# Kernel tuning notes

Measured on AMD Instinct MI355X. Metric: run time of the kernel, lower is better.

Reference implementation:

```python
import jax, jax.numpy as jnp
import numpy as np


def setup_inputs() -> dict:
    key = jax.random.key(0)
    ks = jax.random.split(key, 6)
    B, N, D, C = 16, 4096, 1024, 4
    bags = jax.random.normal(ks[0], (B, N, D), dtype=jnp.float32)
    query = jax.random.normal(ks[1], (D,), dtype=jnp.float32)
    W1 = jax.random.normal(ks[2], (3 * D, 512), dtype=jnp.float32) * 0.02
    b1 = jax.random.normal(ks[3], (512,), dtype=jnp.float32) * 0.02
    W2 = jax.random.normal(ks[4], (512, C), dtype=jnp.float32) * 0.02
    b2 = jax.random.normal(ks[5], (C,), dtype=jnp.float32) * 0.02
    return {"bags": bags, "query": query, "W1": W1, "b1": b1, "W2": W2, "b2": b2}


def reference(bags, query, W1, b1, W2, b2):
    # bags: [B, N, D] instance features (frozen feat_extractor output)
    mean_pool = jnp.mean(bags, axis=1)                     # [B, D]
    max_pool = jnp.max(bags, axis=1)                       # [B, D]
    # attention pooling: softmax over instances of <bag_i, query>
    scores = jax.nn.softmax(jnp.einsum('bnd,d->bn', bags, query), axis=1)  # [B, N]
    attn_pool = jnp.einsum('bn,bnd->bd', scores, bags)     # [B, D]
    x = jnp.concatenate([mean_pool, max_pool, attn_pool], axis=-1)  # [B, 3D]
    x = x @ W1 + b1
    x = x @ W2 + b2
    return x
```

## Files before the change

kernel.cpp:

```cpp
#include <hip/hip_runtime.h>
#include <math.h>

#define BNUM 16
#define NNUM 4096
#define DNUM 1024
#define CNUM 4
#define HNUM 512

#define SCH   64
#define ROWS  (NNUM / SCH)
#define RPW   (ROWS / 4)

#define PSTRIDE 3080
#define NPART   (BNUM * SCH)
#define XOFF    ((size_t)NPART * PSTRIDE)
#define WOFF    (XOFF + (size_t)BNUM * 3 * DNUM)

#define NEG_INF (-__builtin_inff())

__global__ __launch_bounds__(256) void k_mainpass(const float* __restrict__ bags,
                                                  const float* __restrict__ query,
                                                  float* __restrict__ ws) {
    const int chunk = blockIdx.x;
    const int b     = blockIdx.y;
    const int tid   = threadIdx.x;
    const int wave  = tid >> 6;
    const int lane  = tid & 63;

    const float4* q4 = (const float4*)query;
    float4 q[4];
#pragma unroll
    for (int s = 0; s < 4; ++s) q[s] = q4[s * 64 + lane];

    float4 sum[4], mx[4], acc[4];
#pragma unroll
    for (int s = 0; s < 4; ++s) {
        sum[s] = make_float4(0.f, 0.f, 0.f, 0.f);
        acc[s] = make_float4(0.f, 0.f, 0.f, 0.f);
        mx[s]  = make_float4(NEG_INF, NEG_INF, NEG_INF, NEG_INF);
    }
    float m = NEG_INF, l = 0.f;

    const int n0 = chunk * ROWS + wave * RPW;
    const float4* base = (const float4*)(bags + (size_t)b * NNUM * DNUM);

    for (int r = 0; r < RPW; ++r) {
        const float4* row = base + (size_t)(n0 + r) * (DNUM / 4);
        float4 v[4];
#pragma unroll
        for (int s = 0; s < 4; ++s) v[s] = row[s * 64 + lane];

        float pd = 0.f;
#pragma unroll
        for (int s = 0; s < 4; ++s)
            pd += v[s].x * q[s].x + v[s].y * q[s].y + v[s].z * q[s].z + v[s].w * q[s].w;
#pragma unroll
        for (int off = 32; off; off >>= 1) pd += __shfl_xor(pd, off, 64);

        const float mnew  = fmaxf(m, pd);
        const float alpha = __expf(m - mnew);
        const float w     = __expf(pd - mnew);
        l = l * alpha + w;
        m = mnew;

#pragma unroll
        for (int s = 0; s < 4; ++s) {
            sum[s].x += v[s].x; sum[s].y += v[s].y; sum[s].z += v[s].z; sum[s].w += v[s].w;
            mx[s].x = fmaxf(mx[s].x, v[s].x); mx[s].y = fmaxf(mx[s].y, v[s].y);
            mx[s].z = fmaxf(mx[s].z, v[s].z); mx[s].w = fmaxf(mx[s].w, v[s].w);
            acc[s].x = acc[s].x * alpha + w * v[s].x;
            acc[s].y = acc[s].y * alpha + w * v[s].y;
            acc[s].z = acc[s].z * alpha + w * v[s].z;
            acc[s].w = acc[s].w * alpha + w * v[s].w;
        }
    }

    __shared__ float buf[4][DNUM];
    __shared__ float sm[4], sl[4];
    if (lane == 0) { sm[wave] = m; sl[wave] = l; }

    float* wsp = ws + (size_t)(b * SCH + chunk) * PSTRIDE;

#pragma unroll
    for (int s = 0; s < 4; ++s) ((float4*)(&buf[wave][s * 256]))[lane] = sum[s];
    __syncthreads();
    {
        float4 a0 = ((float4*)buf[0])[tid];
        float4 a1 = ((float4*)buf[1])[tid];
        float4 a2 = ((float4*)buf[2])[tid];
        float4 a3 = ((float4*)buf[3])[tid];
        float4 r;
        r.x = a0.x + a1.x + a2.x + a3.x;
        r.y = a0.y + a1.y + a2.y + a3.y;
        r.z = a0.z + a1.z + a2.z + a3.z;
        r.w = a0.w + a1.w + a2.w + a3.w;
        ((float4*)wsp)[tid] = r;
    }
    __syncthreads();

#pragma unroll
    for (int s = 0; s < 4; ++s) ((float4*)(&buf[wave][s * 256]))[lane] = mx[s];
    __syncthreads();
    {
        float4 a0 = ((float4*)buf[0])[tid];
        float4 a1 = ((float4*)buf[1])[tid];
        float4 a2 = ((float4*)buf[2])[tid];
        float4 a3 = ((float4*)buf[3])[tid];
        float4 r;
        r.x = fmaxf(fmaxf(a0.x, a1.x), fmaxf(a2.x, a3.x));
        r.y = fmaxf(fmaxf(a0.y, a1.y), fmaxf(a2.y, a3.y));
        r.z = fmaxf(fmaxf(a0.z, a1.z), fmaxf(a2.z, a3.z));
        r.w = fmaxf(fmaxf(a0.w, a1.w), fmaxf(a2.w, a3.w));
        ((float4*)(wsp + 1024))[tid] = r;
    }
    __syncthreads();

#pragma unroll
    for (int s = 0; s < 4; ++s) ((float4*)(&buf[wave][s * 256]))[lane] = acc[s];
    __syncthreads();
    {
        const float m0 = sm[0], m1 = sm[1], m2 = sm[2], m3 = sm[3];
        const float mb = fmaxf(fmaxf(m0, m1), fmaxf(m2, m3));
        const float e0 = __expf(m0 - mb), e1 = __expf(m1 - mb);
        const float e2 = __expf(m2 - mb), e3 = __expf(m3 - mb);
        float4 a0 = ((float4*)buf[0])[tid];
        float4 a1 = ((float4*)buf[1])[tid];
        float4 a2 = ((float4*)buf[2])[tid];
        float4 a3 = ((float4*)buf[3])[tid];
        float4 r;
        r.x = a0.x * e0 + a1.x * e1 + a2.x * e2 + a3.x * e3;
        r.y = a0.y * e0 + a1.y * e1 + a2.y * e2 + a3.y * e3;
        r.z = a0.z * e0 + a1.z * e1 + a2.z * e2 + a3.z * e3;
        r.w = a0.w * e0 + a1.w * e1 + a2.w * e2 + a3.w * e3;
        ((float4*)(wsp + 2048))[tid] = r;
        if (tid == 0) {
            wsp[3072] = mb;
            wsp[3073] = sl[0] * e0 + sl[1] * e1 + sl[2] * e2 + sl[3] * e3;
        }
    }
}

__global__ __launch_bounds__(64) void k_combine(float* __restrict__ ws) {
    const int b = blockIdx.x;
    const int d = blockIdx.y * 64 + threadIdx.x;
    const float* pb = ws + (size_t)b * SCH * PSTRIDE;

    float mb = NEG_INF;
    for (int c = 0; c < SCH; ++c) mb = fmaxf(mb, pb[(size_t)c * PSTRIDE + 3072]);
    float lb = 0.f;
    for (int c = 0; c < SCH; ++c)
        lb += pb[(size_t)c * PSTRIDE + 3073] * __expf(pb[(size_t)c * PSTRIDE + 3072] - mb);

    float s = 0.f, mxv = NEG_INF, av = 0.f;
    for (int c = 0; c < SCH; ++c) {
        const float* p = pb + (size_t)c * PSTRIDE;
        s += p[d];
        mxv = fmaxf(mxv, p[1024 + d]);
        av += p[2048 + d] * __expf(p[3072] - mb);
    }
    float* x = ws + XOFF + (size_t)b * 3 * DNUM;
    x[d]            = s * (1.f / NNUM);
    x[DNUM + d]     = mxv;
    x[2 * DNUM + d] = av / lb;
}

__global__ __launch_bounds__(256) void k_weff(const float* __restrict__ W1,
                                              const float* __restrict__ W2,
                                              float* __restrict__ ws) {
    const int tid  = threadIdx.x;
    const int wave = tid >> 6, lane = tid & 63;
    const int k    = blockIdx.x * 4 + wave;
    const float*  r  = W1 + (size_t)k * HNUM;
    const float4* w2 = (const float4*)W2;

    float a0 = 0.f, a1 = 0.f, a2 = 0.f, a3 = 0.f;
#pragma unroll
    for (int t = 0; t < 8; ++t) {
        const int j = lane * 8 + t;
        const float  wv = r[j];
        const float4 w  = w2[j];
        a0 += wv * w.x; a1 += wv * w.y; a2 += wv * w.z; a3 += wv * w.w;
    }
#pragma unroll
    for (int off = 32; off; off >>= 1) {
        a0 += __shfl_xor(a0, off, 64);
        a1 += __shfl_xor(a1, off, 64);
        a2 += __shfl_xor(a2, off, 64);
        a3 += __shfl_xor(a3, off, 64);
    }
    if (lane == 0)
        ((float4*)(ws + WOFF))[k] = make_float4(a0, a1, a2, a3);
}

__global__ __launch_bounds__(256) void k_head(const float* __restrict__ b1,
                                              const float* __restrict__ b2,
                                              const float* __restrict__ W2,
                                              const float* __restrict__ ws,
                                              float* __restrict__ out) {
    const int i   = blockIdx.x;
    const int tid = threadIdx.x;
    const float*  x    = ws + XOFF + (size_t)i * 3 * DNUM;
    const float4* weff = (const float4*)(ws + WOFF);
    const float4* w2   = (const float4*)W2;

    float a0 = 0.f, a1 = 0.f, a2 = 0.f, a3 = 0.f;
    for (int k = tid; k < 3 * DNUM; k += 256) {
        const float  xv = x[k];
        const float4 w  = weff[k];
        a0 += xv * w.x; a1 += xv * w.y; a2 += xv * w.z; a3 += xv * w.w;
    }
    for (int j = tid; j < HNUM; j += 256) {
        const float  bv = b1[j];
        const float4 w  = w2[j];
        a0 += bv * w.x; a1 += bv * w.y; a2 += bv * w.z; a3 += bv * w.w;
    }
#pragma unroll
    for (int off = 32; off; off >>= 1) {
        a0 += __shfl_xor(a0, off, 64);
        a1 += __shfl_xor(a1, off, 64);
        a2 += __shfl_xor(a2, off, 64);
        a3 += __shfl_xor(a3, off, 64);
    }
    __shared__ float red[4][4];
    const int wave = tid >> 6, lane = tid & 63;
    if (lane == 0) { red[wave][0] = a0; red[wave][1] = a1; red[wave][2] = a2; red[wave][3] = a3; }
    __syncthreads();
    if (tid < 4) {
        out[i * 4 + tid] = red[0][tid] + red[1][tid] + red[2][tid] + red[3][tid] + b2[tid];
    }
}

extern "C" void kernel_launch(void* const* d_in, const int* in_sizes, int n_in,
                              void* d_out, int out_size, void* d_ws, size_t ws_size,
                              hipStream_t stream) {
    const float* bags  = (const float*)d_in[0];
    const float* query = (const float*)d_in[1];
    const float* W1    = (const float*)d_in[2];
    const float* b1    = (const float*)d_in[3];
    const float* W2    = (const float*)d_in[4];
    const float* b2    = (const float*)d_in[5];
    float* out = (float*)d_out;
    float* ws  = (float*)d_ws;

    k_weff    <<<(3 * DNUM) / 4,        256, 0, stream>>>(W1, W2, ws);
    k_mainpass<<<dim3(SCH, BNUM),       256, 0, stream>>>(bags, query, ws);
    k_combine <<<dim3(BNUM, DNUM / 64),  64, 0, stream>>>(ws);
    k_head    <<<BNUM,                  256, 0, stream>>>(b1, b2, W2, ws, out);
}
```

Before: 405.1 us.

## Process two rows per iteration with lazy rescale; fuse combine and head kernels

The main pass now loads two rows per iteration and rescales the online-softmax accumulators only when the running max increases. This raises memory-level parallelism and removes per-row exp and multiply work. The separate combine and head kernels are merged into one k_finish kernel that reduces the partials and applies the folded weights, saving a launch and a workspace round trip. The b1·W2+b2 bias is precomputed in an extra k_weff block. The fused finish kernel uses only 16 blocks, so its per-bag reduction is less parallel than the old 256-block combine.

```diff
diff --git a/kernel.cpp b/kernel.cpp
--- a/kernel.cpp
+++ b/kernel.cpp
@@ -15,6 +15,7 @@
 #define NPART   (BNUM * SCH)
 #define XOFF    ((size_t)NPART * PSTRIDE)
 #define WOFF    (XOFF + (size_t)BNUM * 3 * DNUM)
+#define BIASOFF (WOFF + (size_t)3 * DNUM * 4)
 
 #define NEG_INF (-__builtin_inff())
 
@@ -44,34 +45,56 @@
     const int n0 = chunk * ROWS + wave * RPW;
     const float4* base = (const float4*)(bags + (size_t)b * NNUM * DNUM);
 
-    for (int r = 0; r < RPW; ++r) {
-        const float4* row = base + (size_t)(n0 + r) * (DNUM / 4);
-        float4 v[4];
-#pragma unroll
-        for (int s = 0; s < 4; ++s) v[s] = row[s * 64 + lane];
-
-        float pd = 0.f;
-#pragma unroll
-        for (int s = 0; s < 4; ++s)
-            pd += v[s].x * q[s].x + v[s].y * q[s].y + v[s].z * q[s].z + v[s].w * q[s].w;
-#pragma unroll
-        for (int off = 32; off; off >>= 1) pd += __shfl_xor(pd, off, 64);
-
-        const float mnew  = fmaxf(m, pd);
-        const float alpha = __expf(m - mnew);
-        const float w     = __expf(pd - mnew);
-        l = l * alpha + w;
-        m = mnew;
-
+    for (int r = 0; r < RPW; r += 2) {
+        const float4* rowA = base + (size_t)(n0 + r) * (DNUM / 4);
+        const float4* rowB = rowA + (DNUM / 4);
+        float4 va[4], vb[4];
+#pragma unroll
+        for (int s = 0; s < 4; ++s) va[s] = rowA[s * 64 + lane];
+#pragma unroll
+        for (int s = 0; s < 4; ++s) vb[s] = rowB[s * 64 + lane];
+
+        float pa = 0.f, pb = 0.f;
 #pragma unroll
         for (int s = 0; s < 4; ++s) {
-            sum[s].x += v[s].x; sum[s].y += v[s].y; sum[s].z += v[s].z; sum[s].w += v[s].w;
-            mx[s].x = fmaxf(mx[s].x, v[s].x); mx[s].y = fmaxf(mx[s].y, v[s].y);
-            mx[s].z = fmaxf(mx[s].z, v[s].z); mx[s].w = fmaxf(mx[s].w, v[s].w);
-            acc[s].x = acc[s].x * alpha + w * v[s].x;
-            acc[s].y = acc[s].y * alpha + w * v[s].y;
-            acc[s].z = acc[s].z * alpha + w * v[s].z;
-            acc[s].w = acc[s].w * alpha + w * v[s].w;
+            pa += va[s].x * q[s].x + va[s].y * q[s].y + va[s].z * q[s].z + va[s].w * q[s].w;
+            pb += vb[s].x * q[s].x + vb[s].y * q[s].y + vb[s].z * q[s].z + vb[s].w * q[s].w;
+        }
+#pragma unroll
+        for (int off = 32; off; off >>= 1) {
+            pa += __shfl_xor(pa, off, 64);
+            pb += __shfl_xor(pb, off, 64);
+        }
+
+        const float mnew = fmaxf(m, fmaxf(pa, pb));
+        if (mnew > m) {
+            const float alpha = __expf(m - mnew);
+            l *= alpha;
+#pragma unroll
+            for (int s = 0; s < 4; ++s) {
+                acc[s].x *= alpha; acc[s].y *= alpha;
+                acc[s].z *= alpha; acc[s].w *= alpha;
+            }
+            m = mnew;
+        }
+        const float wa = __expf(pa - m);
+        const float wb = __expf(pb - m);
+        l += wa + wb;
+
+#pragma unroll
+        for (int s = 0; s < 4; ++s) {
+            sum[s].x += va[s].x + vb[s].x;
+            sum[s].y += va[s].y + vb[s].y;
+            sum[s].z += va[s].z + vb[s].z;
+            sum[s].w += va[s].w + vb[s].w;
+            mx[s].x = fmaxf(mx[s].x, fmaxf(va[s].x, vb[s].x));
+            mx[s].y = fmaxf(mx[s].y, fmaxf(va[s].y, vb[s].y));
+            mx[s].z = fmaxf(mx[s].z, fmaxf(va[s].z, vb[s].z));
+            mx[s].w = fmaxf(mx[s].w, fmaxf(va[s].w, vb[s].w));
+            acc[s].x += wa * va[s].x + wb * vb[s].x;
+            acc[s].y += wa * va[s].y + wb * vb[s].y;
+            acc[s].z += wa * va[s].z + wb * vb[s].z;
+            acc[s].w += wa * va[s].w + wb * vb[s].w;
         }
     }
 
@@ -140,93 +163,138 @@
     }
 }
 
-__global__ __launch_bounds__(64) void k_combine(float* __restrict__ ws) {
-    const int b = blockIdx.x;
-    const int d = blockIdx.y * 64 + threadIdx.x;
-    const float* pb = ws + (size_t)b * SCH * PSTRIDE;
-
-    float mb = NEG_INF;
-    for (int c = 0; c < SCH; ++c) mb = fmaxf(mb, pb[(size_t)c * PSTRIDE + 3072]);
-    float lb = 0.f;
-    for (int c = 0; c < SCH; ++c)
-        lb += pb[(size_t)c * PSTRIDE + 3073] * __expf(pb[(size_t)c * PSTRIDE + 3072] - mb);
-
-    float s = 0.f, mxv = NEG_INF, av = 0.f;
-    for (int c = 0; c < SCH; ++c) {
-        const float* p = pb + (size_t)c * PSTRIDE;
-        s += p[d];
-        mxv = fmaxf(mxv, p[1024 + d]);
-        av += p[2048 + d] * __expf(p[3072] - mb);
-    }
-    float* x = ws + XOFF + (size_t)b * 3 * DNUM;
-    x[d]            = s * (1.f / NNUM);
-    x[DNUM + d]     = mxv;
-    x[2 * DNUM + d] = av / lb;
-}
-
 __global__ __launch_bounds__(256) void k_weff(const float* __restrict__ W1,
                                               const float* __restrict__ W2,
+                                              const float* __restrict__ b1,
+                                              const float* __restrict__ b2,
                                               float* __restrict__ ws) {
     const int tid  = threadIdx.x;
     const int wave = tid >> 6, lane = tid & 63;
-    const int k    = blockIdx.x * 4 + wave;
-    const float*  r  = W1 + (size_t)k * HNUM;
     const float4* w2 = (const float4*)W2;
 
-    float a0 = 0.f, a1 = 0.f, a2 = 0.f, a3 = 0.f;
-#pragma unroll
-    for (int t = 0; t < 8; ++t) {
-        const int j = lane * 8 + t;
-        const float  wv = r[j];
-        const float4 w  = w2[j];
-        a0 += wv * w.x; a1 += wv * w.y; a2 += wv * w.z; a3 += wv * w.w;
+    if (blockIdx.x < 768) {
+        const int k = blockIdx.x * 4 + wave;
+        const float* r = W1 + (size_t)k * HNUM;
+        float a0 = 0.f, a1 = 0.f, a2 = 0.f, a3 = 0.f;
+#pragma unroll
+        for (int t = 0; t < 8; ++t) {
+            const int j = lane * 8 + t;
+            const float  wv = r[j];
+            const float4 w  = w2[j];
+            a0 += wv * w.x; a1 += wv * w.y; a2 += wv * w.z; a3 += wv * w.w;
+        }
+#pragma unroll
+        for (int off = 32; off; off >>= 1) {
+            a0 += __shfl_xor(a0, off, 64);
+            a1 += __shfl_xor(a1, off, 64);
+            a2 += __shfl_xor(a2, off, 64);
+            a3 += __shfl_xor(a3, off, 64);
+        }
+        if (lane == 0)
+            ((float4*)(ws + WOFF))[k] = make_float4(a0, a1, a2, a3);
+    } else if (wave == 0) {
+        float a0 = 0.f, a1 = 0.f, a2 = 0.f, a3 = 0.f;
+#pragma unroll
+        for (int t = 0; t < 8; ++t) {
+            const int j = lane * 8 + t;
+            const float  bv = b1[j];
+            const float4 w  = w2[j];
+            a0 += bv * w.x; a1 += bv * w.y; a2 += bv * w.z; a3 += bv * w.w;
+        }
+#pragma unroll
+        for (int off = 32; off; off >>= 1) {
+            a0 += __shfl_xor(a0, off, 64);
+            a1 += __shfl_xor(a1, off, 64);
+            a2 += __shfl_xor(a2, off, 64);
+            a3 += __shfl_xor(a3, off, 64);
+        }
+        if (lane == 0) {
+            float* bias = ws + BIASOFF;
+            bias[0] = a0 + b2[0];
+            bias[1] = a1 + b2[1];
+            bias[2] = a2 + b2[2];
+            bias[3] = a3 + b2[3];
+        }
+    }
+}
+
+__global__ __launch_bounds__(256) void k_finish(const float* __restrict__ ws,
+                                                float* __restrict__ out) {
+    const int b    = blockIdx.x;
+    const int tid  = threadIdx.x;
+    const int wave = tid >> 6, lane = tid & 63;
+
+    __shared__ float eS[SCH];
+    __shared__ float lbS;
+    __shared__ float red[4][4];
+
+    const float* pb = ws + (size_t)b * SCH * PSTRIDE;
+
+    if (wave == 0) {
+        const float* p = pb + (size_t)lane * PSTRIDE;
+        const float mlane = p[3072];
+        const float llane = p[3073];
+        float mb = mlane;
+#pragma unroll
+        for (int off = 32; off; off >>= 1) mb = fmaxf(mb, __shfl_xor(mb, off, 64));
+        const float e = __expf(mlane - mb);
+        float lb = llane * e;
+#pragma unroll
+        for (int off = 32; off; off >>= 1) lb += __shfl_xor(lb, off, 64);
+        eS[lane] = e;
+        if (lane == 0) lbS = lb;
+    }
+    __syncthreads();
+    const float inv_lb = 1.f / lbS;
+
+    float4 s  = make_float4(0.f, 0.f, 0.f, 0.f);
+    float4 a  = make_float4(0.f, 0.f, 0.f, 0.f);
+    float4 mxv = make_float4(NEG_INF, NEG_INF, NEG_INF, NEG_INF);
+    for (int c = 0; c < SCH; ++c) {
+        const float* p = pb + (size_t)c * PSTRIDE;
+        const float4 sv = ((const float4*)p)[tid];
+        const float4 mv = ((const float4*)(p + 1024))[tid];
+        const float4 av = ((const float4*)(p + 2048))[tid];
+        const float e = eS[c];
+        s.x += sv.x; s.y += sv.y; s.z += sv.z; s.w += sv.w;
+        mxv.x = fmaxf(mxv.x, mv.x); mxv.y = fmaxf(mxv.y, mv.y);
+        mxv.z = fmaxf(mxv.z, mv.z); mxv.w = fmaxf(mxv.w, mv.w);
+        a.x += e * av.x; a.y += e * av.y; a.z += e * av.z; a.w += e * av.w;
+    }
+
+    const float4* weff = (const float4*)(ws + WOFF);
+    float c0 = 0.f, c1 = 0.f, c2 = 0.f, c3 = 0.f;
+    const float scm = 1.f / NNUM;
+    const float xm[4] = { s.x * scm, s.y * scm, s.z * scm, s.w * scm };
+    const float xx[4] = { mxv.x, mxv.y, mxv.z, mxv.w };
+    const float xa[4] = { a.x * inv_lb, a.y * inv_lb, a.z * inv_lb, a.w * inv_lb };
+#pragma unroll
+    for (int k = 0; k < 4; ++k) {
+        const float4 w = weff[tid * 4 + k];
+        c0 += xm[k] * w.x; c1 += xm[k] * w.y; c2 += xm[k] * w.z; c3 += xm[k] * w.w;
+    }
+#pragma unroll
+    for (int k = 0; k < 4; ++k) {
+        const float4 w = weff[DNUM + tid * 4 + k];
+        c0 += xx[k] * w.x; c1 += xx[k] * w.y; c2 += xx[k] * w.z; c3 += xx[k] * w.w;
+    }
+#pragma unroll
+    for (int k = 0; k < 4; ++k) {
+        const float4 w = weff[2 * DNUM + tid * 4 + k];
+        c0 += xa[k] * w.x; c1 += xa[k] * w.y; c2 += xa[k] * w.z; c3 += xa[k] * w.w;
     }
 #pragma unroll
     for (int off = 32; off; off >>= 1) {
-        a0 += __shfl_xor(a0, off, 64);
-        a1 += __shfl_xor(a1, off, 64);
-        a2 += __shfl_xor(a2, off, 64);
-        a3 += __shfl_xor(a3, off, 64);
-    }
-    if (lane == 0)
-        ((float4*)(ws + WOFF))[k] = make_float4(a0, a1, a2, a3);
-}
-
-__global__ __launch_bounds__(256) void k_head(const float* __restrict__ b1,
-                                              const float* __restrict__ b2,
-                                              const float* __restrict__ W2,
-                                              const float* __restrict__ ws,
-                                              float* __restrict__ out) {
-    const int i   = blockIdx.x;
-    const int tid = threadIdx.x;
-    const float*  x    = ws + XOFF + (size_t)i * 3 * DNUM;
-    const float4* weff = (const float4*)(ws + WOFF);
-    const float4* w2   = (const float4*)W2;
-
-    float a0 = 0.f, a1 = 0.f, a2 = 0.f, a3 = 0.f;
-    for (int k = tid; k < 3 * DNUM; k += 256) {
-        const float  xv = x[k];
-        const float4 w  = weff[k];
-        a0 += xv * w.x; a1 += xv * w.y; a2 += xv * w.z; a3 += xv * w.w;
-    }
-    for (int j = tid; j < HNUM; j += 256) {
-        const float  bv = b1[j];
-        const float4 w  = w2[j];
-        a0 += bv * w.x; a1 += bv * w.y; a2 += bv * w.z; a3 += bv * w.w;
-    }
-#pragma unroll
-    for (int off = 32; off; off >>= 1) {
-        a0 += __shfl_xor(a0, off, 64);
-        a1 += __shfl_xor(a1, off, 64);
-        a2 += __shfl_xor(a2, off, 64);
-        a3 += __shfl_xor(a3, off, 64);
-    }
-    __shared__ float red[4][4];
-    const int wave = tid >> 6, lane = tid & 63;
-    if (lane == 0) { red[wave][0] = a0; red[wave][1] = a1; red[wave][2] = a2; red[wave][3] = a3; }
+        c0 += __shfl_xor(c0, off, 64);
+        c1 += __shfl_xor(c1, off, 64);
+        c2 += __shfl_xor(c2, off, 64);
+        c3 += __shfl_xor(c3, off, 64);
+    }
+    if (lane == 0) { red[wave][0] = c0; red[wave][1] = c1; red[wave][2] = c2; red[wave][3] = c3; }
     __syncthreads();
     if (tid < 4) {
-        out[i * 4 + tid] = red[0][tid] + red[1][tid] + red[2][tid] + red[3][tid] + b2[tid];
+        const float* bias = ws + BIASOFF;
+        out[b * 4 + tid] = red[0][tid] + red[1][tid] + red[2][tid] + red[3][tid] + bias[tid];
     }
 }
 
@@ -242,8 +310,7 @@
     float* out = (float*)d_out;
     float* ws  = (float*)d_ws;
 
-    k_weff    <<<(3 * DNUM) / 4,        256, 0, stream>>>(W1, W2, ws);
-    k_mainpass<<<dim3(SCH, BNUM),       256, 0, stream>>>(bags, query, ws);
-    k_combine <<<dim3(BNUM, DNUM / 64),  64, 0, stream>>>(ws);
-    k_head    <<<BNUM,                  256, 0, stream>>>(b1, b2, W2, ws, out);
+    k_weff    <<<769,             256, 0, stream>>>(W1, W2, b1, b2, ws);
+    k_mainpass<<<dim3(SCH, BNUM), 256, 0, stream>>>(bags, query, ws);
+    k_finish  <<<BNUM,            256, 0, stream>>>(ws, out);
 }
```

After: 393.3 us. 2.9% less time.
